# Performance work log

Measured on AMD Instinct MI355X. Metric: run time of the kernel, lower is better.

Reference implementation:

```python
import jax, jax.numpy as jnp
import numpy as np

N = 50000        # nodes
E = 800000       # edges (before self-loops)
F_IN = 128       # input node features
HID = 64         # GAT hidden per head
HEADS1 = 4
NUM_GRAPHS = 64
NEG_SLOPE = 0.2  # PyG GATConv default leaky_relu slope


def setup_inputs() -> dict:
    key = jax.random.key(0)
    ks = jax.random.split(key, 12)
    x = jax.random.normal(ks[0], (N, F_IN), dtype=jnp.float32)
    edge_index = jax.random.randint(ks[1], (2, E), 0, N, dtype=jnp.int32)
    batch = jnp.sort(jax.random.randint(ks[2], (N,), 0, NUM_GRAPHS, dtype=jnp.int32))
    s = 1.0 / np.sqrt(F_IN)
    W1 = jax.random.uniform(ks[3], (F_IN, HEADS1 * HID), jnp.float32, -s, s)
    att_src1 = jax.random.uniform(ks[4], (HEADS1, HID), jnp.float32, -s, s)
    att_dst1 = jax.random.uniform(ks[5], (HEADS1, HID), jnp.float32, -s, s)
    b1 = jnp.zeros((HEADS1 * HID,), jnp.float32)
    s2 = 1.0 / np.sqrt(HEADS1 * HID)
    W2 = jax.random.uniform(ks[6], (HEADS1 * HID, HID), jnp.float32, -s2, s2)
    att_src2 = jax.random.uniform(ks[7], (1, HID), jnp.float32, -s2, s2)
    att_dst2 = jax.random.uniform(ks[8], (1, HID), jnp.float32, -s2, s2)
    b2 = jnp.zeros((HID,), jnp.float32)
    return {"x": x, "edge_index": edge_index, "batch": batch,
            "W1": W1, "att_src1": att_src1, "att_dst1": att_dst1, "b1": b1,
            "W2": W2, "att_src2": att_src2, "att_dst2": att_dst2, "b2": b2}


def gat_conv(x, src, dst, W, a_src, a_dst, bias, heads, out_dim):
    # PyG GATConv: h = x @ W (no lin bias); per-node attention logits;
    # e_ij = leaky_relu(alpha_src[j] + alpha_dst[i]); softmax over dst groups;
    # out_i = sum_j alpha_ij * h_j; concat heads; + bias.
    n = x.shape[0]
    h = (x @ W).reshape(n, heads, out_dim)                 # [N,H,C]
    alpha_src = jnp.einsum('nhc,hc->nh', h, a_src)         # [N,H]
    alpha_dst = jnp.einsum('nhc,hc->nh', h, a_dst)         # [N,H]
    e = jax.nn.leaky_relu(alpha_src[src] + alpha_dst[dst], NEG_SLOPE)  # [E,H]
    m = jax.ops.segment_max(e, dst, num_segments=n)        # segment softmax (stable)
    e = jnp.exp(e - m[dst])
    denom = jax.ops.segment_sum(e, dst, num_segments=n)
    alpha = e / denom[dst]                                 # [E,H]
    msg = h[src] * alpha[:, :, None]                       # [E,H,C]
    agg = jax.ops.segment_sum(msg, dst, num_segments=n)    # [N,H,C]
    return agg.reshape(n, heads * out_dim) + bias


def reference(x, edge_index, batch, W1, att_src1, att_dst1, b1, W2, att_src2, att_dst2, b2):
    # add self loops (PyG GATConv default add_self_loops=True)
    loops = jnp.arange(N, dtype=edge_index.dtype)
    src = jnp.concatenate([edge_index[0], loops])
    dst = jnp.concatenate([edge_index[1], loops])
    h = jax.nn.relu(gat_conv(x, src, dst, W1, att_src1, att_dst1, b1, HEADS1, HID))
    h = gat_conv(h, src, dst, W2, att_src2, att_dst2, b2, 1, HID)
    # global mean pool over graphs
    sums = jax.ops.segment_sum(h, batch, num_segments=NUM_GRAPHS)
    cnt = jax.ops.segment_sum(jnp.ones((N,), h.dtype), batch, num_segments=NUM_GRAPHS)
    return sums / jnp.maximum(cnt, 1.0)[:, None]
```

## Files before the change

### kernel.cpp

```cpp
#include <hip/hip_runtime.h>
#include <math.h>


typedef unsigned short ushort_t;
typedef __bf16 bf16x8 __attribute__((ext_vector_type(8)));
typedef float  f32x4  __attribute__((ext_vector_type(4)));

__device__ inline float bf2f(ushort_t u) { return __uint_as_float((unsigned)u << 16); }
__device__ inline ushort_t f2bf(float x) {
  unsigned b = __float_as_uint(x);
  return (ushort_t)((b + 0x7fff + ((b >> 16) & 1)) >> 16);
}
__device__ inline float leaky(float v) { return (v > 0.f) ? v : 0.2f * v; }

__device__ inline f32x4 mfma16(bf16x8 a, bf16x8 b, f32x4 c) {
  return __builtin_amdgcn_mfma_f32_16x16x32_bf16(a, b, c, 0, 0, 0);
}

__device__ inline void packB_one(const float* __restrict__ B, ushort_t* __restrict__ bh,
                                 ushort_t* __restrict__ bl, int K, int Nn, int t) {
  int KT = K >> 5;
  int l = t & 63, fb = t >> 6;
  int nt = fb / KT, kt = fb - nt * KT;
  int col = nt * 16 + (l & 15);
  int k0 = kt * 32 + (l >> 4) * 8;
  ushort_t h[8], lo[8];
  #pragma unroll
  for (int j = 0; j < 8; ++j) {
    float v = B[(size_t)(k0 + j) * Nn + col];
    h[j] = f2bf(v);
    lo[j] = f2bf(v - bf2f(h[j]));
  }
  size_t o = (size_t)t * 8;
  *(ushort4*)(bh + o)     = make_ushort4(h[0], h[1], h[2], h[3]);
  *(ushort4*)(bh + o + 4) = make_ushort4(h[4], h[5], h[6], h[7]);
  *(ushort4*)(bl + o)     = make_ushort4(lo[0], lo[1], lo[2], lo[3]);
  *(ushort4*)(bl + o + 4) = make_ushort4(lo[4], lo[5], lo[6], lo[7]);
}

__global__ void k_setup(const int* __restrict__ edst, int E, int* __restrict__ deg,
                        const int* __restrict__ batch, int N, int G,
                        int* __restrict__ gstart,
                        const float* __restrict__ W1, const float* __restrict__ W2,
                        ushort_t* __restrict__ B1h, ushort_t* __restrict__ B1l,
                        ushort_t* __restrict__ B2h, ushort_t* __restrict__ B2l,
                        int HB, int GBB) {
  int b = blockIdx.x, tid = threadIdx.x;
  if (b < HB) {
    int i = b * 256 + tid;
    if (i < E) atomicAdd(&deg[edst[i]], 1);
  } else if (b < HB + GBB) {
    int i = (b - HB) * 256 + tid;
    if (i < N) {
      int bb = batch[i];
      int bp = (i == 0) ? -1 : batch[i - 1];
      for (int g = bp + 1; g <= bb; ++g) gstart[g] = i;
      if (i == N - 1)
        for (int g = bb + 1; g <= G; ++g) gstart[g] = N;
    }
  } else {
    int t = (b - HB - GBB) * 256 + tid;
    if (t < 4096) packB_one(W1, B1h, B1l, 128, 256, t);
    else if (t < 6144) packB_one(W2, B2h, B2l, 256, 64, t - 4096);
  }
}

__global__ void k_scan_bsum(const int* __restrict__ deg, int n, int* __restrict__ bsum) {
  __shared__ int ws[16];
  int tid = threadIdx.x, lane = tid & 63, wv = tid >> 6;
  int i = blockIdx.x * 1024 + tid;
  int v = (i < n) ? deg[i] + 1 : 0;
  #pragma unroll
  for (int off = 1; off < 64; off <<= 1) v += __shfl_xor(v, off);
  if (lane == 0) ws[wv] = v;
  __syncthreads();
  if (tid < 16) {
    int s = ws[tid];
    #pragma unroll
    for (int off = 1; off < 16; off <<= 1) s += __shfl_xor(s, off);
    if (tid == 0) bsum[blockIdx.x] = s;
  }
}

__global__ void k_scan_bbase(const int* __restrict__ bsum, int nb,
                             int* __restrict__ bbase, int* __restrict__ offsets, int n) {
  int lane = threadIdx.x & 63;
  int v = (lane < nb) ? bsum[lane] : 0;
  int x = v;
  #pragma unroll
  for (int off = 1; off < 64; off <<= 1) {
    int t = __shfl_up(x, off);
    if (lane >= off) x += t;
  }
  if (lane < nb) bbase[lane] = x - v;
  if (lane == nb - 1) offsets[n] = x;
}

__global__ void k_scan_final(const int* __restrict__ deg, int n,
                             const int* __restrict__ bbase,
                             int* __restrict__ offsets, int* __restrict__ cursor) {
  __shared__ int wsum[16];
  int tid = threadIdx.x, lane = tid & 63, wv = tid >> 6;
  int i = blockIdx.x * 1024 + tid;
  int v = (i < n) ? deg[i] + 1 : 0;
  int x = v;
  #pragma unroll
  for (int off = 1; off < 64; off <<= 1) {
    int t = __shfl_up(x, off);
    if (lane >= off) x += t;
  }
  if (lane == 63) wsum[wv] = x;
  __syncthreads();
  if (wv == 0 && lane < 16) {
    int s = wsum[lane];
    #pragma unroll
    for (int off = 1; off < 16; off <<= 1) {
      int t = __shfl_up(s, off);
      if (lane >= off) s += t;
    }
    wsum[lane] = s;
  }
  __syncthreads();
  int wbase = (wv == 0) ? 0 : wsum[wv - 1];
  int incl = bbase[blockIdx.x] + wbase + x;
  if (i < n) { int o = incl - v; offsets[i] = o; cursor[i] = o; }
}

template<int KT, int TERMS, int WM>
__device__ void gemm_att_body(int bx, int by,
                              const float* __restrict__ Af32, const ushort_t* __restrict__ Ah,
                              const ushort_t* __restrict__ Bh, const ushort_t* __restrict__ Bl,
                              const float* __restrict__ a_srcW, const float* __restrict__ a_dstW,
                              ushort_t* __restrict__ hb, float* __restrict__ as_,
                              float* __restrict__ ad_, int M, int Nn, int H) {
  const int tid = threadIdx.x;
  const int w = tid >> 6, lane = tid & 63;
  const int wm = w & (WM - 1), wn = w / WM;
  const int m0w = bx * (WM * 32) + wm * 32;
  const int n0  = by * ((4 / WM) * 64) + wn * 64;
  const int head = n0 >> 6;
  const int mt0 = m0w >> 4, nt0 = n0 >> 4;

  const float* pX[2];
  int rowmi[2];
  const ushort_t* pAh[2];
  #pragma unroll
  for (int mi = 0; mi < 2; ++mi) {
    if constexpr (TERMS == 3) {
      rowmi[mi] = (mt0 + mi) * 16 + (lane & 15);
      pX[mi] = Af32 + (size_t)rowmi[mi] * (KT * 32) + ((lane >> 4) << 3);
    } else {
      size_t fa = (size_t)(mt0 + mi) * KT;
      pAh[mi] = Ah + fa * 512 + (size_t)lane * 8;
    }
  }
  const ushort_t* pBh[4];
  const ushort_t* pBl[4];
  #pragma unroll
  for (int ni = 0; ni < 4; ++ni) {
    size_t fb = (size_t)(nt0 + ni) * KT;
    pBh[ni] = Bh + fb * 512 + (size_t)lane * 8;
    pBl[ni] = Bl + fb * 512 + (size_t)lane * 8;
  }

  f32x4 acc[2][4];
  #pragma unroll
  for (int mi = 0; mi < 2; ++mi)
    #pragma unroll
    for (int ni = 0; ni < 4; ++ni)
      acc[mi][ni] = (f32x4){0.f, 0.f, 0.f, 0.f};

  for (int kt = 0; kt < KT; ++kt) {
    const size_t ko = (size_t)kt * 512;
    bf16x8 ahf[2], alf[2], bhf[4], blf[4];
    #pragma unroll
    for (int mi = 0; mi < 2; ++mi) {
      if constexpr (TERMS == 3) {
        float v[8] = {0.f, 0.f, 0.f, 0.f, 0.f, 0.f, 0.f, 0.f};
        if (rowmi[mi] < M) {
          float4 a = *(const float4*)(pX[mi] + kt * 32);
          float4 b = *(const float4*)(pX[mi] + kt * 32 + 4);
          v[0] = a.x; v[1] = a.y; v[2] = a.z; v[3] = a.w;
          v[4] = b.x; v[5] = b.y; v[6] = b.z; v[7] = b.w;
        }
        union { ushort_t u[8]; bf16x8 f; } uh, ul;
        #pragma unroll
        for (int j = 0; j < 8; ++j) {
          uh.u[j] = f2bf(v[j]);
          ul.u[j] = f2bf(v[j] - bf2f(uh.u[j]));
        }
        ahf[mi] = uh.f;
        alf[mi] = ul.f;
      } else {
        ahf[mi] = *(const bf16x8*)(pAh[mi] + ko);
      }
    }
    #pragma unroll
    for (int ni = 0; ni < 4; ++ni) {
      bhf[ni] = *(const bf16x8*)(pBh[ni] + ko);
      blf[ni] = *(const bf16x8*)(pBl[ni] + ko);
    }
    #pragma unroll
    for (int mi = 0; mi < 2; ++mi)
      #pragma unroll
      for (int ni = 0; ni < 4; ++ni) {
        if constexpr (TERMS == 3)
          acc[mi][ni] = mfma16(alf[mi], bhf[ni], acc[mi][ni]);
        acc[mi][ni] = mfma16(ahf[mi], blf[ni], acc[mi][ni]);
        acc[mi][ni] = mfma16(ahf[mi], bhf[ni], acc[mi][ni]);
      }
  }

  const int c16 = lane & 15, q = lane >> 4;
  float sv[4], dv[4];
  #pragma unroll
  for (int ni = 0; ni < 4; ++ni) {
    sv[ni] = a_srcW[head * 64 + ni * 16 + c16];
    dv[ni] = a_dstW[head * 64 + ni * 16 + c16];
  }
  #pragma unroll
  for (int mi = 0; mi < 2; ++mi) {
    #pragma unroll
    for (int r = 0; r < 4; ++r) {
      int gr = m0w + mi * 16 + q * 4 + r;
      float ps = acc[mi][0][r] * sv[0] + acc[mi][1][r] * sv[1] +
                 acc[mi][2][r] * sv[2] + acc[mi][3][r] * sv[3];
      float pd = acc[mi][0][r] * dv[0] + acc[mi][1][r] * dv[1] +
                 acc[mi][2][r] * dv[2] + acc[mi][3][r] * dv[3];
      #pragma unroll
      for (int off = 1; off < 16; off <<= 1) {
        ps += __shfl_xor(ps, off);
        pd += __shfl_xor(pd, off);
      }
      if (gr < M) {
        #pragma unroll
        for (int ni = 0; ni < 4; ++ni)
          hb[(size_t)gr * Nn + n0 + ni * 16 + c16] = f2bf(acc[mi][ni][r]);
        if (c16 == 0) { as_[gr * H + head] = ps; ad_[gr * H + head] = pd; }
      }
    }
  }
}

__global__ __launch_bounds__(256)
void k_scatter_gemm1(const int* __restrict__ esrc, const int* __restrict__ edst,
                     int E, int N, int* __restrict__ cursor, int2* __restrict__ sed,
                     int SCB,
                     const float* __restrict__ x,
                     const ushort_t* __restrict__ B1h, const ushort_t* __restrict__ B1l,
                     const float* __restrict__ as_w, const float* __restrict__ ad_w,
                     ushort_t* __restrict__ h1b, float* __restrict__ as1,
                     float* __restrict__ ad1, int GB1) {
  if (blockIdx.x < SCB) {
    int i = blockIdx.x * 256 + threadIdx.x;
    int EE = E + N;
    if (i < EE) {
      int d, s;
      if (i < E) { d = edst[i]; s = esrc[i]; }
      else       { d = i - E;   s = i - E;   }
      int pos = atomicAdd(&cursor[d], 1);
      sed[pos] = make_int2(s, d);
    }
  } else {
    int b = blockIdx.x - SCB;
    gemm_att_body<4, 3, 2>(b % GB1, b / GB1, x, nullptr, B1h, B1l,
                           as_w, ad_w, h1b, as1, ad1, N, 256, 4);
  }
}

__global__ __launch_bounds__(256)
void k_gemm2(const ushort_t* __restrict__ A2h,
             const ushort_t* __restrict__ B2h, const ushort_t* __restrict__ B2l,
             const float* __restrict__ as_w, const float* __restrict__ ad_w,
             ushort_t* __restrict__ h2b, float* __restrict__ as2,
             float* __restrict__ ad2, int M) {
  gemm_att_body<8, 2, 4>(blockIdx.x, 0, nullptr, A2h, B2h, B2l,
                         as_w, ad_w, h2b, as2, ad2, M, 64, 1);
}

__global__ void k_edgew1(const int2* __restrict__ sed, const float* __restrict__ as1,
                         const float* __restrict__ ad1, float* __restrict__ w1, int EE) {
  int t = blockIdx.x * blockDim.x + threadIdx.x;
  if (t >= EE * 4) return;
  int e = t >> 2, h = t & 3;
  int2 p = sed[e];
  w1[t] = __expf(leaky(as1[p.x * 4 + h] + ad1[p.y * 4 + h]));
}

__global__ void k_edgew2(const int2* __restrict__ sed, const float* __restrict__ as2,
                         const float* __restrict__ ad2, float* __restrict__ w2, int EE) {
  int e = blockIdx.x * blockDim.x + threadIdx.x;
  if (e >= EE) return;
  int2 p = sed[e];
  w2[e] = __expf(leaky(as2[p.x] + ad2[p.y]));
}

__global__ void k_agg1(const ushort_t* __restrict__ h1b, const float* __restrict__ w1,
                       const int* __restrict__ offs, const int2* __restrict__ sed,
                       const float* __restrict__ b1, ushort_t* __restrict__ a2h, int N) {
  int gt = blockIdx.x * blockDim.x + threadIdx.x;
  int wid = gt >> 6, lane = gt & 63;
  if (wid >= N) return;
  int head = lane >> 4, sub = lane & 15, coff = sub << 2;
  int start = offs[wid], end = offs[wid + 1];

  float denom = 0.f;
  float4 acc = make_float4(0.f, 0.f, 0.f, 0.f);
  int e = start;
  for (; e + 8 <= end; e += 8) {
    int s0 = sed[e].x, s1 = sed[e + 1].x, s2 = sed[e + 2].x, s3 = sed[e + 3].x;
    int s4 = sed[e + 4].x, s5 = sed[e + 5].x, s6 = sed[e + 6].x, s7 = sed[e + 7].x;
    float wa = w1[(e + 0) * 4 + head], wb = w1[(e + 1) * 4 + head];
    float wc = w1[(e + 2) * 4 + head], wd = w1[(e + 3) * 4 + head];
    float we = w1[(e + 4) * 4 + head], wf = w1[(e + 5) * 4 + head];
    float wg = w1[(e + 6) * 4 + head], wh = w1[(e + 7) * 4 + head];
    ushort4 g0 = *(const ushort4*)(h1b + (size_t)s0 * 256 + head * 64 + coff);
    ushort4 g1 = *(const ushort4*)(h1b + (size_t)s1 * 256 + head * 64 + coff);
    ushort4 g2 = *(const ushort4*)(h1b + (size_t)s2 * 256 + head * 64 + coff);
    ushort4 g3 = *(const ushort4*)(h1b + (size_t)s3 * 256 + head * 64 + coff);
    ushort4 g4 = *(const ushort4*)(h1b + (size_t)s4 * 256 + head * 64 + coff);
    ushort4 g5 = *(const ushort4*)(h1b + (size_t)s5 * 256 + head * 64 + coff);
    ushort4 g6 = *(const ushort4*)(h1b + (size_t)s6 * 256 + head * 64 + coff);
    ushort4 g7 = *(const ushort4*)(h1b + (size_t)s7 * 256 + head * 64 + coff);
    denom += ((wa + wb) + (wc + wd)) + ((we + wf) + (wg + wh));
    acc.x += wa * bf2f(g0.x) + wb * bf2f(g1.x) + wc * bf2f(g2.x) + wd * bf2f(g3.x)
           + we * bf2f(g4.x) + wf * bf2f(g5.x) + wg * bf2f(g6.x) + wh * bf2f(g7.x);
    acc.y += wa * bf2f(g0.y) + wb * bf2f(g1.y) + wc * bf2f(g2.y) + wd * bf2f(g3.y)
           + we * bf2f(g4.y) + wf * bf2f(g5.y) + wg * bf2f(g6.y) + wh * bf2f(g7.y);
    acc.z += wa * bf2f(g0.z) + wb * bf2f(g1.z) + wc * bf2f(g2.z) + wd * bf2f(g3.z)
           + we * bf2f(g4.z) + wf * bf2f(g5.z) + wg * bf2f(g6.z) + wh * bf2f(g7.z);
    acc.w += wa * bf2f(g0.w) + wb * bf2f(g1.w) + wc * bf2f(g2.w) + wd * bf2f(g3.w)
           + we * bf2f(g4.w) + wf * bf2f(g5.w) + wg * bf2f(g6.w) + wh * bf2f(g7.w);
  }
  for (; e + 4 <= end; e += 4) {
    int s0 = sed[e].x, s1 = sed[e + 1].x, s2 = sed[e + 2].x, s3 = sed[e + 3].x;
    float wa = w1[(e + 0) * 4 + head], wb = w1[(e + 1) * 4 + head];
    float wc = w1[(e + 2) * 4 + head], wd = w1[(e + 3) * 4 + head];
    ushort4 g0 = *(const ushort4*)(h1b + (size_t)s0 * 256 + head * 64 + coff);
    ushort4 g1 = *(const ushort4*)(h1b + (size_t)s1 * 256 + head * 64 + coff);
    ushort4 g2 = *(const ushort4*)(h1b + (size_t)s2 * 256 + head * 64 + coff);
    ushort4 g3 = *(const ushort4*)(h1b + (size_t)s3 * 256 + head * 64 + coff);
    denom += (wa + wb) + (wc + wd);
    acc.x += wa * bf2f(g0.x) + wb * bf2f(g1.x) + wc * bf2f(g2.x) + wd * bf2f(g3.x);
    acc.y += wa * bf2f(g0.y) + wb * bf2f(g1.y) + wc * bf2f(g2.y) + wd * bf2f(g3.y);
    acc.z += wa * bf2f(g0.z) + wb * bf2f(g1.z) + wc * bf2f(g2.z) + wd * bf2f(g3.z);
    acc.w += wa * bf2f(g0.w) + wb * bf2f(g1.w) + wc * bf2f(g2.w) + wd * bf2f(g3.w);
  }
  for (; e < end; ++e) {
    int s = sed[e].x;
    float w = w1[e * 4 + head];
    ushort4 g = *(const ushort4*)(h1b + (size_t)s * 256 + head * 64 + coff);
    denom += w;
    acc.x += w * bf2f(g.x); acc.y += w * bf2f(g.y);
    acc.z += w * bf2f(g.z); acc.w += w * bf2f(g.w);
  }
  float inv = 1.f / denom;
  float4 bv = *(const float4*)(b1 + head * 64 + coff);
  int c0 = head * 64 + coff;
  int fa = (wid >> 4) * 8 + (c0 >> 5);
  int fl = (wid & 15) | (((c0 >> 3) & 3) << 4);
  size_t addr = ((size_t)fa * 64 + fl) * 8 + (c0 & 7);
  ushort4 o;
  o.x = f2bf(fmaxf(acc.x * inv + bv.x, 0.f));
  o.y = f2bf(fmaxf(acc.y * inv + bv.y, 0.f));
  o.z = f2bf(fmaxf(acc.z * inv + bv.z, 0.f));
  o.w = f2bf(fmaxf(acc.w * inv + bv.w, 0.f));
  *(ushort4*)(a2h + addr) = o;
}

__global__ void k_agg2(const ushort_t* __restrict__ h2b, const float* __restrict__ w2,
                       const int* __restrict__ offs, const int2* __restrict__ sed,
                       const float* __restrict__ b2, float* __restrict__ hfin, int N) {
  int gt = blockIdx.x * blockDim.x + threadIdx.x;
  int wid = gt >> 6, lane = gt & 63;
  if (wid >= N) return;
  int half = lane >> 5, li = lane & 31;
  int start = offs[wid], end = offs[wid + 1];

  float dn = 0.f, acc0 = 0.f, acc1 = 0.f;
  int e = start;
  for (; e + 8 <= end; e += 8) {
    int e0 = e + half, e1 = e + 2 + half, e2 = e + 4 + half, e3 = e + 6 + half;
    int s0 = sed[e0].x, s1 = sed[e1].x, s2 = sed[e2].x, s3 = sed[e3].x;
    float wa = w2[e0], wb = w2[e1], wc = w2[e2], wd = w2[e3];
    unsigned g0 = *(const unsigned*)(h2b + (size_t)s0 * 64 + li * 2);
    unsigned g1 = *(const unsigned*)(h2b + (size_t)s1 * 64 + li * 2);
    unsigned g2 = *(const unsigned*)(h2b + (size_t)s2 * 64 + li * 2);
    unsigned g3 = *(const unsigned*)(h2b + (size_t)s3 * 64 + li * 2);
    dn += (wa + wb) + (wc + wd);
    acc0 += wa * __uint_as_float(g0 << 16) + wb * __uint_as_float(g1 << 16)
          + wc * __uint_as_float(g2 << 16) + wd * __uint_as_float(g3 << 16);
    acc1 += wa * __uint_as_float(g0 & 0xffff0000u) + wb * __uint_as_float(g1 & 0xffff0000u)
          + wc * __uint_as_float(g2 & 0xffff0000u) + wd * __uint_as_float(g3 & 0xffff0000u);
  }
  for (; e + 2 <= end; e += 2) {
    int e0 = e + half;
    int s0 = sed[e0].x;
    float wa = w2[e0];
    unsigned g0 = *(const unsigned*)(h2b + (size_t)s0 * 64 + li * 2);
    dn += wa;
    acc0 += wa * __uint_as_float(g0 << 16);
    acc1 += wa * __uint_as_float(g0 & 0xffff0000u);
  }
  if (e < end && half == 0) {
    int s0 = sed[e].x;
    float wa = w2[e];
    unsigned g0 = *(const unsigned*)(h2b + (size_t)s0 * 64 + li * 2);
    dn += wa;
    acc0 += wa * __uint_as_float(g0 << 16);
    acc1 += wa * __uint_as_float(g0 & 0xffff0000u);
  }
  acc0 += __shfl_xor(acc0, 32);
  acc1 += __shfl_xor(acc1, 32);
  dn   += __shfl_xor(dn, 32);
  if (half == 0) {
    float inv = 1.f / dn;
    float2 bv = *(const float2*)(b2 + li * 2);
    float2 o;
    o.x = acc0 * inv + bv.x;
    o.y = acc1 * inv + bv.y;
    *(float2*)(hfin + (size_t)wid * 64 + li * 2) = o;
  }
}

__global__ void k_pool(const float* __restrict__ hfin, const int* __restrict__ gstart,
                       float* __restrict__ out) {
  int g = blockIdx.x;
  int c = threadIdx.x & 63, r = threadIdx.x >> 6;
  int start = gstart[g], cnt = gstart[g + 1] - start;
  float acc = 0.f;
  for (int i = r; i < cnt; i += 4)
    acc += hfin[(size_t)(start + i) * 64 + c];
  __shared__ float red[256];
  red[threadIdx.x] = acc;
  __syncthreads();
  if (r == 0)
    out[g * 64 + c] = (red[c] + red[64 + c] + red[128 + c] + red[192 + c]) /
                      fmaxf((float)cnt, 1.f);
}

extern "C" void kernel_launch(void* const* d_in, const int* in_sizes, int n_in,
                              void* d_out, int out_size, void* d_ws, size_t ws_size,
                              hipStream_t stream) {
  const float* x        = (const float*)d_in[0];
  const int*   ei       = (const int*)d_in[1];
  const int*   batch    = (const int*)d_in[2];
  const float* W1       = (const float*)d_in[3];
  const float* att_src1 = (const float*)d_in[4];
  const float* att_dst1 = (const float*)d_in[5];
  const float* b1       = (const float*)d_in[6];
  const float* W2       = (const float*)d_in[7];
  const float* att_src2 = (const float*)d_in[8];
  const float* att_dst2 = (const float*)d_in[9];
  const float* b2       = (const float*)d_in[10];
  float* out = (float*)d_out;

  const int N = in_sizes[0] / 128;
  const int E = in_sizes[1] / 2;
  const int EE = E + N;
  const int* esrc = ei;
  const int* edst = ei + E;

  const int GB2 = (N + 127) / 128;
  const int GB1 = GB2 * 2;
  const int MF  = GB2 * 8;
  const int NB  = (N + 1023) / 1024;
  const int HB  = (E + 255) / 256;
  const int GBB = (N + 255) / 256;
  const int SCB = (EE + 255) / 256;

  char* p = (char*)d_ws;
  auto alloc = [&](size_t bytes) -> void* {
    void* r = (void*)p;
    p += (bytes + 255) & ~(size_t)255;
    return r;
  };
  ushort_t* A2h  = (ushort_t*)alloc((size_t)MF * 8 * 64 * 16);
  ushort_t* B1h  = (ushort_t*)alloc((size_t)16 * 4 * 64 * 16);
  ushort_t* B1l  = (ushort_t*)alloc((size_t)16 * 4 * 64 * 16);
  ushort_t* B2h  = (ushort_t*)alloc((size_t)4 * 8 * 64 * 16);
  ushort_t* B2l  = (ushort_t*)alloc((size_t)4 * 8 * 64 * 16);
  ushort_t* h1b  = (ushort_t*)alloc((size_t)N * 256 * 2);
  ushort_t* h2b  = (ushort_t*)alloc((size_t)N * 64 * 2);
  float*    hfin = (float*)alloc((size_t)N * 64 * 4);
  float*    as1  = (float*)alloc((size_t)N * 4 * 4);
  float*    ad1  = (float*)alloc((size_t)N * 4 * 4);
  float*    as2  = (float*)alloc((size_t)N * 4);
  float*    ad2  = (float*)alloc((size_t)N * 4);
  float*    w1   = (float*)alloc((size_t)EE * 4 * 4);
  float*    w2   = (float*)alloc((size_t)EE * 4);
  int*  deg     = (int*)alloc((size_t)N * 4);
  int*  offsets = (int*)alloc((size_t)(N + 1) * 4);
  int*  cursor  = (int*)alloc((size_t)N * 4);
  int2* sed     = (int2*)alloc((size_t)EE * 8);
  int*  bsum    = (int*)alloc(64 * 4);
  int*  bbase   = (int*)alloc(64 * 4);
  int*  gstart  = (int*)alloc(65 * 4);

  hipMemsetAsync(deg, 0, (size_t)N * 4, stream);

  k_setup<<<HB + GBB + 24, 256, 0, stream>>>(edst, E, deg, batch, N, 64, gstart,
                                             W1, W2, B1h, B1l, B2h, B2l, HB, GBB);

  k_scan_bsum<<<NB, 1024, 0, stream>>>(deg, N, bsum);
  k_scan_bbase<<<1, 64, 0, stream>>>(bsum, NB, bbase, offsets, N);
  k_scan_final<<<NB, 1024, 0, stream>>>(deg, N, bbase, offsets, cursor);

  k_scatter_gemm1<<<SCB + GB1 * 2, 256, 0, stream>>>(
      esrc, edst, E, N, cursor, sed, SCB,
      x, B1h, B1l, att_src1, att_dst1, h1b, as1, ad1, GB1);

  k_edgew1<<<(EE * 4 + 255) / 256, 256, 0, stream>>>(sed, as1, ad1, w1, EE);
  int wave_blocks = (N * 64 + 255) / 256;
  k_agg1<<<wave_blocks, 256, 0, stream>>>(h1b, w1, offsets, sed, b1, A2h, N);

  k_gemm2<<<GB2, 256, 0, stream>>>(A2h, B2h, B2l, att_src2, att_dst2,
                                   h2b, as2, ad2, N);
  k_edgew2<<<(EE + 255) / 256, 256, 0, stream>>>(sed, as2, ad2, w2, EE);
  k_agg2<<<wave_blocks, 256, 0, stream>>>(h2b, w2, offsets, sed, b2, hfin, N);

  k_pool<<<64, 256, 0, stream>>>(hfin, gstart, out);
}
```

Measured before the change: 317.1 us.

## Fuse edge-weight computation into aggregation kernels and split scatter from GEMM1

```diff
diff --git a/kernel.cpp b/kernel.cpp
--- a/kernel.cpp
+++ b/kernel.cpp
@@ -124,6 +124,20 @@
   int wbase = (wv == 0) ? 0 : wsum[wv - 1];
   int incl = bbase[blockIdx.x] + wbase + x;
   if (i < n) { int o = incl - v; offsets[i] = o; cursor[i] = o; }
+}
+
+__global__ void k_scatter(const int* __restrict__ esrc, const int* __restrict__ edst,
+                          int E, int N, int* __restrict__ cursor,
+                          int2* __restrict__ sed) {
+  int stride = gridDim.x * blockDim.x;
+  int EE = E + N;
+  for (int i = blockIdx.x * blockDim.x + threadIdx.x; i < EE; i += stride) {
+    int d, s;
+    if (i < E) { d = edst[i]; s = esrc[i]; }
+    else       { d = i - E;   s = i - E;   }
+    int pos = atomicAdd(&cursor[d], 1);
+    sed[pos] = make_int2(s, d);
+  }
 }
 
 template<int KT, int TERMS, int WM>
@@ -243,29 +257,13 @@
 }
 
 __global__ __launch_bounds__(256)
-void k_scatter_gemm1(const int* __restrict__ esrc, const int* __restrict__ edst,
-                     int E, int N, int* __restrict__ cursor, int2* __restrict__ sed,
-                     int SCB,
-                     const float* __restrict__ x,
-                     const ushort_t* __restrict__ B1h, const ushort_t* __restrict__ B1l,
-                     const float* __restrict__ as_w, const float* __restrict__ ad_w,
-                     ushort_t* __restrict__ h1b, float* __restrict__ as1,
-                     float* __restrict__ ad1, int GB1) {
-  if (blockIdx.x < SCB) {
-    int i = blockIdx.x * 256 + threadIdx.x;
-    int EE = E + N;
-    if (i < EE) {
-      int d, s;
-      if (i < E) { d = edst[i]; s = esrc[i]; }
-      else       { d = i - E;   s = i - E;   }
-      int pos = atomicAdd(&cursor[d], 1);
-      sed[pos] = make_int2(s, d);
-    }
-  } else {
-    int b = blockIdx.x - SCB;
-    gemm_att_body<4, 3, 2>(b % GB1, b / GB1, x, nullptr, B1h, B1l,
-                           as_w, ad_w, h1b, as1, ad1, N, 256, 4);
-  }
+void k_gemm1(const float* __restrict__ x,
+             const ushort_t* __restrict__ B1h, const ushort_t* __restrict__ B1l,
+             const float* __restrict__ as_w, const float* __restrict__ ad_w,
+             ushort_t* __restrict__ h1b, float* __restrict__ as1,
+             float* __restrict__ ad1, int M) {
+  gemm_att_body<4, 3, 2>(blockIdx.x, blockIdx.y, x, nullptr, B1h, B1l,
+                         as_w, ad_w, h1b, as1, ad1, M, 256, 4);
 }
 
 __global__ __launch_bounds__(256)
@@ -278,77 +276,61 @@
                          as_w, ad_w, h2b, as2, ad2, M, 64, 1);
 }
 
-__global__ void k_edgew1(const int2* __restrict__ sed, const float* __restrict__ as1,
-                         const float* __restrict__ ad1, float* __restrict__ w1, int EE) {
-  int t = blockIdx.x * blockDim.x + threadIdx.x;
-  if (t >= EE * 4) return;
-  int e = t >> 2, h = t & 3;
-  int2 p = sed[e];
-  w1[t] = __expf(leaky(as1[p.x * 4 + h] + ad1[p.y * 4 + h]));
-}
-
-__global__ void k_edgew2(const int2* __restrict__ sed, const float* __restrict__ as2,
-                         const float* __restrict__ ad2, float* __restrict__ w2, int EE) {
-  int e = blockIdx.x * blockDim.x + threadIdx.x;
-  if (e >= EE) return;
-  int2 p = sed[e];
-  w2[e] = __expf(leaky(as2[p.x] + ad2[p.y]));
-}
-
-__global__ void k_agg1(const ushort_t* __restrict__ h1b, const float* __restrict__ w1,
-                       const int* __restrict__ offs, const int2* __restrict__ sed,
-                       const float* __restrict__ b1, ushort_t* __restrict__ a2h, int N) {
+__global__ void k_agg1(const ushort_t* __restrict__ h1b, const float* __restrict__ as1,
+                       const float* __restrict__ ad1, const int* __restrict__ offs,
+                       const int2* __restrict__ sed, const float* __restrict__ b1,
+                       ushort_t* __restrict__ a2h, int N) {
   int gt = blockIdx.x * blockDim.x + threadIdx.x;
   int wid = gt >> 6, lane = gt & 63;
   if (wid >= N) return;
   int head = lane >> 4, sub = lane & 15, coff = sub << 2;
   int start = offs[wid], end = offs[wid + 1];
+  float ad = ad1[wid * 4 + head];
 
   float denom = 0.f;
   float4 acc = make_float4(0.f, 0.f, 0.f, 0.f);
   int e = start;
   for (; e + 8 <= end; e += 8) {
-    int s0 = sed[e].x, s1 = sed[e + 1].x, s2 = sed[e + 2].x, s3 = sed[e + 3].x;
-    int s4 = sed[e + 4].x, s5 = sed[e + 5].x, s6 = sed[e + 6].x, s7 = sed[e + 7].x;
-    float wa = w1[(e + 0) * 4 + head], wb = w1[(e + 1) * 4 + head];
-    float wc = w1[(e + 2) * 4 + head], wd = w1[(e + 3) * 4 + head];
-    float we = w1[(e + 4) * 4 + head], wf = w1[(e + 5) * 4 + head];
-    float wg = w1[(e + 6) * 4 + head], wh = w1[(e + 7) * 4 + head];
-    ushort4 g0 = *(const ushort4*)(h1b + (size_t)s0 * 256 + head * 64 + coff);
-    ushort4 g1 = *(const ushort4*)(h1b + (size_t)s1 * 256 + head * 64 + coff);
-    ushort4 g2 = *(const ushort4*)(h1b + (size_t)s2 * 256 + head * 64 + coff);
-    ushort4 g3 = *(const ushort4*)(h1b + (size_t)s3 * 256 + head * 64 + coff);
-    ushort4 g4 = *(const ushort4*)(h1b + (size_t)s4 * 256 + head * 64 + coff);
-    ushort4 g5 = *(const ushort4*)(h1b + (size_t)s5 * 256 + head * 64 + coff);
-    ushort4 g6 = *(const ushort4*)(h1b + (size_t)s6 * 256 + head * 64 + coff);
-    ushort4 g7 = *(const ushort4*)(h1b + (size_t)s7 * 256 + head * 64 + coff);
-    denom += ((wa + wb) + (wc + wd)) + ((we + wf) + (wg + wh));
-    acc.x += wa * bf2f(g0.x) + wb * bf2f(g1.x) + wc * bf2f(g2.x) + wd * bf2f(g3.x)
-           + we * bf2f(g4.x) + wf * bf2f(g5.x) + wg * bf2f(g6.x) + wh * bf2f(g7.x);
-    acc.y += wa * bf2f(g0.y) + wb * bf2f(g1.y) + wc * bf2f(g2.y) + wd * bf2f(g3.y)
-           + we * bf2f(g4.y) + wf * bf2f(g5.y) + wg * bf2f(g6.y) + wh * bf2f(g7.y);
-    acc.z += wa * bf2f(g0.z) + wb * bf2f(g1.z) + wc * bf2f(g2.z) + wd * bf2f(g3.z)
-           + we * bf2f(g4.z) + wf * bf2f(g5.z) + wg * bf2f(g6.z) + wh * bf2f(g7.z);
-    acc.w += wa * bf2f(g0.w) + wb * bf2f(g1.w) + wc * bf2f(g2.w) + wd * bf2f(g3.w)
-           + we * bf2f(g4.w) + wf * bf2f(g5.w) + wg * bf2f(g6.w) + wh * bf2f(g7.w);
+    int s[8]; float w[8]; ushort4 g[8];
+    #pragma unroll
+    for (int j = 0; j < 8; ++j) s[j] = sed[e + j].x;
+    #pragma unroll
+    for (int j = 0; j < 8; ++j)
+      g[j] = *(const ushort4*)(h1b + (size_t)s[j] * 256 + head * 64 + coff);
+    #pragma unroll
+    for (int j = 0; j < 8; ++j)
+      w[j] = __expf(leaky(as1[s[j] * 4 + head] + ad));
+    #pragma unroll
+    for (int j = 0; j < 8; ++j) {
+      denom += w[j];
+      acc.x += w[j] * bf2f(g[j].x);
+      acc.y += w[j] * bf2f(g[j].y);
+      acc.z += w[j] * bf2f(g[j].z);
+      acc.w += w[j] * bf2f(g[j].w);
+    }
   }
   for (; e + 4 <= end; e += 4) {
-    int s0 = sed[e].x, s1 = sed[e + 1].x, s2 = sed[e + 2].x, s3 = sed[e + 3].x;
-    float wa = w1[(e + 0) * 4 + head], wb = w1[(e + 1) * 4 + head];
-    float wc = w1[(e + 2) * 4 + head], wd = w1[(e + 3) * 4 + head];
-    ushort4 g0 = *(const ushort4*)(h1b + (size_t)s0 * 256 + head * 64 + coff);
-    ushort4 g1 = *(const ushort4*)(h1b + (size_t)s1 * 256 + head * 64 + coff);
-    ushort4 g2 = *(const ushort4*)(h1b + (size_t)s2 * 256 + head * 64 + coff);
-    ushort4 g3 = *(const ushort4*)(h1b + (size_t)s3 * 256 + head * 64 + coff);
-    denom += (wa + wb) + (wc + wd);
-    acc.x += wa * bf2f(g0.x) + wb * bf2f(g1.x) + wc * bf2f(g2.x) + wd * bf2f(g3.x);
-    acc.y += wa * bf2f(g0.y) + wb * bf2f(g1.y) + wc * bf2f(g2.y) + wd * bf2f(g3.y);
-    acc.z += wa * bf2f(g0.z) + wb * bf2f(g1.z) + wc * bf2f(g2.z) + wd * bf2f(g3.z);
-    acc.w += wa * bf2f(g0.w) + wb * bf2f(g1.w) + wc * bf2f(g2.w) + wd * bf2f(g3.w);
+    int s[4]; float w[4]; ushort4 g[4];
+    #pragma unroll
+    for (int j = 0; j < 4; ++j) s[j] = sed[e + j].x;
+    #pragma unroll
+    for (int j = 0; j < 4; ++j)
+      g[j] = *(const ushort4*)(h1b + (size_t)s[j] * 256 + head * 64 + coff);
+    #pragma unroll
+    for (int j = 0; j < 4; ++j)
+      w[j] = __expf(leaky(as1[s[j] * 4 + head] + ad));
+    #pragma unroll
+    for (int j = 0; j < 4; ++j) {
+      denom += w[j];
+      acc.x += w[j] * bf2f(g[j].x);
+      acc.y += w[j] * bf2f(g[j].y);
+      acc.z += w[j] * bf2f(g[j].z);
+      acc.w += w[j] * bf2f(g[j].w);
+    }
   }
   for (; e < end; ++e) {
     int s = sed[e].x;
-    float w = w1[e * 4 + head];
+    float w = __expf(leaky(as1[s * 4 + head] + ad));
     ushort4 g = *(const ushort4*)(h1b + (size_t)s * 256 + head * 64 + coff);
     denom += w;
     acc.x += w * bf2f(g.x); acc.y += w * bf2f(g.y);
@@ -368,25 +350,30 @@
   *(ushort4*)(a2h + addr) = o;
 }
 
-__global__ void k_agg2(const ushort_t* __restrict__ h2b, const float* __restrict__ w2,
-                       const int* __restrict__ offs, const int2* __restrict__ sed,
-                       const float* __restrict__ b2, float* __restrict__ hfin, int N) {
+__global__ void k_agg2(const ushort_t* __restrict__ h2b, const float* __restrict__ as2,
+                       const float* __restrict__ ad2, const int* __restrict__ offs,
+                       const int2* __restrict__ sed, const float* __restrict__ b2,
+                       float* __restrict__ hfin, int N) {
   int gt = blockIdx.x * blockDim.x + threadIdx.x;
   int wid = gt >> 6, lane = gt & 63;
   if (wid >= N) return;
   int half = lane >> 5, li = lane & 31;
   int start = offs[wid], end = offs[wid + 1];
+  float ad = ad2[wid];
 
   float dn = 0.f, acc0 = 0.f, acc1 = 0.f;
   int e = start;
   for (; e + 8 <= end; e += 8) {
     int e0 = e + half, e1 = e + 2 + half, e2 = e + 4 + half, e3 = e + 6 + half;
     int s0 = sed[e0].x, s1 = sed[e1].x, s2 = sed[e2].x, s3 = sed[e3].x;
-    float wa = w2[e0], wb = w2[e1], wc = w2[e2], wd = w2[e3];
     unsigned g0 = *(const unsigned*)(h2b + (size_t)s0 * 64 + li * 2);
     unsigned g1 = *(const unsigned*)(h2b + (size_t)s1 * 64 + li * 2);
     unsigned g2 = *(const unsigned*)(h2b + (size_t)s2 * 64 + li * 2);
     unsigned g3 = *(const unsigned*)(h2b + (size_t)s3 * 64 + li * 2);
+    float wa = __expf(leaky(as2[s0] + ad));
+    float wb = __expf(leaky(as2[s1] + ad));
+    float wc = __expf(leaky(as2[s2] + ad));
+    float wd = __expf(leaky(as2[s3] + ad));
     dn += (wa + wb) + (wc + wd);
     acc0 += wa * __uint_as_float(g0 << 16) + wb * __uint_as_float(g1 << 16)
           + wc * __uint_as_float(g2 << 16) + wd * __uint_as_float(g3 << 16);
@@ -396,7 +383,7 @@
   for (; e + 2 <= end; e += 2) {
     int e0 = e + half;
     int s0 = sed[e0].x;
-    float wa = w2[e0];
+    float wa = __expf(leaky(as2[s0] + ad));
     unsigned g0 = *(const unsigned*)(h2b + (size_t)s0 * 64 + li * 2);
     dn += wa;
     acc0 += wa * __uint_as_float(g0 << 16);
@@ -404,7 +391,7 @@
   }
   if (e < end && half == 0) {
     int s0 = sed[e].x;
-    float wa = w2[e];
+    float wa = __expf(leaky(as2[s0] + ad));
     unsigned g0 = *(const unsigned*)(h2b + (size_t)s0 * 64 + li * 2);
     dn += wa;
     acc0 += wa * __uint_as_float(g0 << 16);
@@ -467,7 +454,6 @@
   const int NB  = (N + 1023) / 1024;
   const int HB  = (E + 255) / 256;
   const int GBB = (N + 255) / 256;
-  const int SCB = (EE + 255) / 256;
 
   char* p = (char*)d_ws;
   auto alloc = [&](size_t bytes) -> void* {
@@ -487,8 +473,6 @@
   float*    ad1  = (float*)alloc((size_t)N * 4 * 4);
   float*    as2  = (float*)alloc((size_t)N * 4);
   float*    ad2  = (float*)alloc((size_t)N * 4);
-  float*    w1   = (float*)alloc((size_t)EE * 4 * 4);
-  float*    w2   = (float*)alloc((size_t)EE * 4);
   int*  deg     = (int*)alloc((size_t)N * 4);
   int*  offsets = (int*)alloc((size_t)(N + 1) * 4);
   int*  cursor  = (int*)alloc((size_t)N * 4);
@@ -506,18 +490,16 @@
   k_scan_bbase<<<1, 64, 0, stream>>>(bsum, NB, bbase, offsets, N);
   k_scan_final<<<NB, 1024, 0, stream>>>(deg, N, bbase, offsets, cursor);
 
-  k_scatter_gemm1<<<SCB + GB1 * 2, 256, 0, stream>>>(
-      esrc, edst, E, N, cursor, sed, SCB,
-      x, B1h, B1l, att_src1, att_dst1, h1b, as1, ad1, GB1);
-
-  k_edgew1<<<(EE * 4 + 255) / 256, 256, 0, stream>>>(sed, as1, ad1, w1, EE);
+  k_scatter<<<1024, 256, 0, stream>>>(esrc, edst, E, N, cursor, sed);
+
+  k_gemm1<<<dim3(GB1, 2), 256, 0, stream>>>(x, B1h, B1l, att_src1, att_dst1,
+                                            h1b, as1, ad1, N);
   int wave_blocks = (N * 64 + 255) / 256;
-  k_agg1<<<wave_blocks, 256, 0, stream>>>(h1b, w1, offsets, sed, b1, A2h, N);
+  k_agg1<<<wave_blocks, 256, 0, stream>>>(h1b, as1, ad1, offsets, sed, b1, A2h, N);
 
   k_gemm2<<<GB2, 256, 0, stream>>>(A2h, B2h, B2l, att_src2, att_dst2,
                                    h2b, as2, ad2, N);
-  k_edgew2<<<(EE + 255) / 256, 256, 0, stream>>>(sed, as2, ad2, w2, EE);
-  k_agg2<<<wave_blocks, 256, 0, stream>>>(h2b, w2, offsets, sed, b2, hfin, N);
+  k_agg2<<<wave_blocks, 256, 0, stream>>>(h2b, as2, ad2, offsets, sed, b2, hfin, N);
 
   k_pool<<<64, 256, 0, stream>>>(hfin, gstart, out);
 }
```

Result: faster. 302.6 us (-4.6%).
